# Kernel optimization log

Hardware: AMD Instinct MI355X
Metric: run time of the kernel (lower is better)

## Reference

```python
import jax, jax.numpy as jnp
import numpy as np

N_POINTS = 1440   # number of detector angles (thetas)
N_INT = 4000      # trapezoid integration samples along each ray
N_GRID = 4096     # SoS field is (N_GRID, N_GRID)
GRID_LO, GRID_HI = -0.06, 0.06
R_BODY = 0.05
V0 = 1500.0


def setup_inputs() -> dict:
    key = jax.random.key(0)
    k1, k2, k3 = jax.random.split(key, 3)
    # query point strictly inside the body circle (r < R_body)
    x = jnp.float32(0.012)
    y = jnp.float32(-0.007)
    # speed-of-sound field ~ water SoS with heterogeneity, strictly positive
    SoS = (1480.0 + 40.0 * jax.random.uniform(k3, (N_GRID, N_GRID))).astype(jnp.float32)
    thetas = jnp.linspace(0.0, 2.0 * jnp.pi, N_POINTS, dtype=jnp.float32).reshape(-1, 1)
    steps = jnp.linspace(0.0, 1.0, N_INT, dtype=jnp.float32).reshape(1, -1)
    x_vec = jnp.linspace(GRID_LO, GRID_HI, N_GRID, dtype=jnp.float32)
    dx = x_vec[1] - x_vec[0]
    return {
        "x": x, "y": y, "SoS": SoS,
        "thetas": thetas, "steps": steps,
        "x0": x_vec[0], "y0": x_vec[0], "dx": dx, "dy": dx,
        "R_body": jnp.float32(R_BODY), "v0": jnp.float32(V0),
    }


def reference(x, y, SoS, thetas, steps, x0, y0, dx, dy, R_body, v0):
    # polar coords of query point; note torch code uses atan2(x, y)
    r = jnp.sqrt(x * x + y * y)
    phi = jnp.arctan2(x, y)
    s = r * jnp.sin(thetas - phi)                      # (P,1)
    arg = jnp.maximum(R_body * R_body - s * s, 0.0)    # shared, >0 when r<R_body
    sqrt_arg = jnp.sqrt(arg)
    l_in = sqrt_arg + r * jnp.cos(thetas - phi)
    l_out = 2.0 * sqrt_arg * (jnp.cos(phi - thetas) >= 0.0).astype(sqrt_arg.dtype)
    l = jnp.where(r < R_body, l_in, l_out)             # (P,1) chord lengths

    xs = l * steps                                     # (P,N) arc-length samples
    px = x - xs * jnp.sin(thetas)                      # (P,N) sample positions
    py = y - xs * jnp.cos(thetas)
    x_index = jnp.round((px - x0) / dx).astype(jnp.int32)
    y_index = jnp.round((py - y0) / dy).astype(jnp.int32)
    # gather: negative row index (-y_index) wraps from the end, as in torch/numpy
    vals = 1.0 - v0 / SoS[-y_index, x_index]           # (P,N)
    # trapezoid over non-uniformly labeled x = l*steps (uniform per row)
    dseg = jnp.diff(xs, axis=1)                        # (P,N-1)
    wf = jnp.sum(0.5 * (vals[:, :-1] + vals[:, 1:]) * dseg, axis=1)
    return thetas.reshape(-1), wf
```

## Files before the change

kernel.cpp:

```cpp
#include <hip/hip_runtime.h>

#define N_POINTS 1440
#define N_INT    4000
#define N_GRID   4096

__global__ __launch_bounds__(256) void wavefront_sos_kernel(
    const float* __restrict__ xp,
    const float* __restrict__ yp,
    const float* __restrict__ SoS,
    const float* __restrict__ thetas,
    const float* __restrict__ steps,
    const float* __restrict__ x0p,
    const float* __restrict__ y0p,
    const float* __restrict__ dxp,
    const float* __restrict__ dyp,
    const float* __restrict__ Rp,
    const float* __restrict__ v0p,
    float* __restrict__ out)
{
    const int p = blockIdx.x;

    const float x  = xp[0];
    const float y  = yp[0];
    const float x0 = x0p[0];
    const float y0 = y0p[0];
    const float dx = dxp[0];
    const float dy = dyp[0];
    const float Rb = Rp[0];
    const float v0 = v0p[0];

    const float theta = thetas[p];

    const float r   = sqrtf(x * x + y * y);
    const float phi = atan2f(x, y);
    const float st  = sinf(theta);
    const float ct  = cosf(theta);

    const float s       = r * sinf(theta - phi);
    const float arg     = fmaxf(Rb * Rb - s * s, 0.0f);
    const float sq      = sqrtf(arg);
    const float l_in    = sq + r * cosf(theta - phi);
    const float l_out   = 2.0f * sq * (cosf(phi - theta) >= 0.0f ? 1.0f : 0.0f);
    const float l       = (r < Rb) ? l_in : l_out;

    float acc = 0.0f;
    for (int j = threadIdx.x; j < N_INT; j += blockDim.x) {
        const float sj = steps[j];
        const float s_next = (j + 1 < N_INT) ? steps[j + 1] : steps[N_INT - 1];
        const float s_prev = (j > 0)         ? steps[j - 1] : steps[0];
        const float w = 0.5f * (s_next - s_prev);

        const float xs = l * sj;
        const float px = x - xs * st;
        const float py = y - xs * ct;

        const int xi = (int)rintf((px - x0) / dx);
        const int yi = (int)rintf((py - y0) / dy);

        const int row = (-yi) & (N_GRID - 1);
        const int col = xi & (N_GRID - 1);

        const float v = 1.0f - v0 / SoS[row * N_GRID + col];
        acc += w * v;
    }

    for (int off = 32; off > 0; off >>= 1)
        acc += __shfl_down(acc, off, 64);

    __shared__ float wave_sums[4];
    const int lane = threadIdx.x & 63;
    const int wave = threadIdx.x >> 6;
    if (lane == 0) wave_sums[wave] = acc;
    __syncthreads();

    if (threadIdx.x == 0) {
        const float total = wave_sums[0] + wave_sums[1] + wave_sums[2] + wave_sums[3];
        out[p] = theta;
        out[N_POINTS + p] = l * total;
    }
}

extern "C" void kernel_launch(void* const* d_in, const int* in_sizes, int n_in,
                              void* d_out, int out_size, void* d_ws, size_t ws_size,
                              hipStream_t stream) {
    (void)in_sizes; (void)n_in; (void)out_size; (void)d_ws; (void)ws_size;

    const float* xp     = (const float*)d_in[0];
    const float* yp     = (const float*)d_in[1];
    const float* SoS    = (const float*)d_in[2];
    const float* thetas = (const float*)d_in[3];
    const float* steps  = (const float*)d_in[4];
    const float* x0p    = (const float*)d_in[5];
    const float* y0p    = (const float*)d_in[6];
    const float* dxp    = (const float*)d_in[7];
    const float* dyp    = (const float*)d_in[8];
    const float* Rp     = (const float*)d_in[9];
    const float* v0p    = (const float*)d_in[10];

    float* out = (float*)d_out;

    wavefront_sos_kernel<<<N_POINTS, 256, 0, stream>>>(
        xp, yp, SoS, thetas, steps, x0p, y0p, dxp, dyp, Rp, v0p, out);
}
```

Before: 128.4 us.

## Precompute affine index coefficients, unroll sample loop, swizzle block-to-angle mapping

Folds the per-sample position and grid-index arithmetic into one FMA per axis by precomputing affine coefficients, which removes two divisions per sample. The division by SoS becomes a hardware reciprocal. The main loop is fully unrolled with a separate tail for the remainder. Blocks are remapped so that consecutive block IDs cover angles spread across the range, meant to change gather locality across CUs and caches. Rounding can differ at pixel boundaries because of the reassociated arithmetic and the approximate reciprocal, which may slightly change results.

```diff
diff --git a/kernel.cpp b/kernel.cpp
--- a/kernel.cpp
+++ b/kernel.cpp
@@ -3,6 +3,9 @@
 #define N_POINTS 1440
 #define N_INT    4000
 #define N_GRID   4096
+#define BLOCK    256
+#define MAIN_ITERS (N_INT / BLOCK)
+#define REMAIN     (N_INT - MAIN_ITERS * BLOCK)
 
 __global__ __launch_bounds__(256) void wavefront_sos_kernel(
     const float* __restrict__ xp,
@@ -18,7 +21,8 @@
     const float* __restrict__ v0p,
     float* __restrict__ out)
 {
-    const int p = blockIdx.x;
+    const int b = blockIdx.x;
+    const int p = (b & 7) * (N_POINTS / 8) + (b >> 3);
 
     const float x  = xp[0];
     const float y  = yp[0];
@@ -36,32 +40,57 @@
     const float st  = sinf(theta);
     const float ct  = cosf(theta);
 
-    const float s       = r * sinf(theta - phi);
-    const float arg     = fmaxf(Rb * Rb - s * s, 0.0f);
-    const float sq      = sqrtf(arg);
-    const float l_in    = sq + r * cosf(theta - phi);
-    const float l_out   = 2.0f * sq * (cosf(phi - theta) >= 0.0f ? 1.0f : 0.0f);
-    const float l       = (r < Rb) ? l_in : l_out;
+    const float s     = r * sinf(theta - phi);
+    const float arg   = fmaxf(Rb * Rb - s * s, 0.0f);
+    const float sq    = sqrtf(arg);
+    const float l_in  = sq + r * cosf(theta - phi);
+    const float l_out = 2.0f * sq * (cosf(phi - theta) >= 0.0f ? 1.0f : 0.0f);
+    const float l     = (r < Rb) ? l_in : l_out;
+
+    const float Ax = (x - x0) / dx;
+    const float Bx = l * st / dx;
+    const float Ay = (y - y0) / dy;
+    const float By = l * ct / dy;
 
     float acc = 0.0f;
-    for (int j = threadIdx.x; j < N_INT; j += blockDim.x) {
+
+#pragma unroll
+    for (int it = 0; it < MAIN_ITERS; ++it) {
+        const int j = threadIdx.x + it * BLOCK;
         const float sj = steps[j];
-        const float s_next = (j + 1 < N_INT) ? steps[j + 1] : steps[N_INT - 1];
-        const float s_prev = (j > 0)         ? steps[j - 1] : steps[0];
-        const float w = 0.5f * (s_next - s_prev);
+        const float sn = steps[j + 1];
+        const float sp = (j > 0) ? steps[j - 1] : steps[0];
+        const float w  = 0.5f * (sn - sp);
 
-        const float xs = l * sj;
-        const float px = x - xs * st;
-        const float py = y - xs * ct;
-
-        const int xi = (int)rintf((px - x0) / dx);
-        const int yi = (int)rintf((py - y0) / dy);
-
+        const float fx = fmaf(sj, -Bx, Ax);
+        const float fy = fmaf(sj, -By, Ay);
+        const int xi = (int)rintf(fx);
+        const int yi = (int)rintf(fy);
         const int row = (-yi) & (N_GRID - 1);
         const int col = xi & (N_GRID - 1);
 
-        const float v = 1.0f - v0 / SoS[row * N_GRID + col];
-        acc += w * v;
+        const float sosv = SoS[row * N_GRID + col];
+        const float v = 1.0f - v0 * __builtin_amdgcn_rcpf(sosv);
+        acc = fmaf(w, v, acc);
+    }
+
+    if (threadIdx.x < REMAIN) {
+        const int j = MAIN_ITERS * BLOCK + threadIdx.x;
+        const float sj = steps[j];
+        const float sn = (j + 1 < N_INT) ? steps[j + 1] : steps[N_INT - 1];
+        const float sp = steps[j - 1];
+        const float w  = 0.5f * (sn - sp);
+
+        const float fx = fmaf(sj, -Bx, Ax);
+        const float fy = fmaf(sj, -By, Ay);
+        const int xi = (int)rintf(fx);
+        const int yi = (int)rintf(fy);
+        const int row = (-yi) & (N_GRID - 1);
+        const int col = xi & (N_GRID - 1);
+
+        const float sosv = SoS[row * N_GRID + col];
+        const float v = 1.0f - v0 * __builtin_amdgcn_rcpf(sosv);
+        acc = fmaf(w, v, acc);
     }
 
     for (int off = 32; off > 0; off >>= 1)
@@ -99,6 +128,6 @@
 
     float* out = (float*)d_out;
 
-    wavefront_sos_kernel<<<N_POINTS, 256, 0, stream>>>(
+    wavefront_sos_kernel<<<N_POINTS, BLOCK, 0, stream>>>(
         xp, yp, SoS, thetas, steps, x0p, y0p, dxp, dyp, Rp, v0p, out);
 }
```

Measured after the change: 120.9 us. 1.06x faster.
